# Kernel optimization log

Hardware: AMD Instinct MI355X
Metric: run time of the kernel (lower is better)

## Reference

```python
import jax, jax.numpy as jnp
import numpy as np


def setup_inputs() -> dict:
    key = jax.random.key(0)
    ks = jax.random.split(key, 6)
    B, N, F = 32, 1000, 256
    x = jax.random.normal(ks[0], (B, N, F), jnp.float32)
    num_nodes = jax.random.randint(ks[1], (B,), 500, N + 1, dtype=jnp.int32)
    num_sentences = jax.random.randint(ks[2], (B,), 10, 100, dtype=jnp.int32)
    valid = (jnp.arange(N)[None, :] < num_nodes[:, None]).astype(jnp.float32)
    # sparse-like weighted adjacency (avg degree ~20), zeroed on padded rows/cols
    w = jax.random.uniform(ks[3], (B, N, N), jnp.float32)
    m = (jax.random.uniform(ks[4], (B, N, N)) < 0.02).astype(jnp.float32)
    adj = w * m * valid[:, :, None] * valid[:, None, :]
    W = jax.random.normal(ks[5], (F, 1), jnp.float32) * 0.1
    b = jnp.zeros((1,), jnp.float32)
    return dict(x=x, adj=adj, W=W, b=b, num_nodes=num_nodes,
                num_sentences=num_sentences, num_output_sentences=3)


def reference(x, adj, W, b, num_nodes, num_sentences, num_output_sentences):
    B, N, F = x.shape
    I = jnp.eye(N, dtype=x.dtype)
    valid = jnp.arange(N)[None, :] < num_nodes[:, None]  # [B,N]

    # --- GCNConv attention: sym-normalized (A_bin + I), out dim 1 ---
    A_bin = (adj > 0).astype(x.dtype)
    A_hat = A_bin + I
    dis = A_hat.sum(-1) ** -0.5  # deg >= 1 from self loops
    norm = dis[:, :, None] * A_hat * dis[:, None, :]
    alpha = jnp.einsum('bnm,bmf,fo->bno', norm, x, W)[..., 0] + b[0]
    alpha = jax.nn.sigmoid(alpha ** 2)           # pow(.,2) then sigmoid
    alpha = jnp.where(valid, alpha, -1.0)        # padded nodes sort last, cut to 0

    # --- top-k cutoff: keep highest-alpha nodes until num_output_sentences
    # sentence nodes (node index < num_sentences) have been seen ---
    order = jnp.argsort(-alpha, axis=-1)                      # descending
    is_sent = (order < num_sentences[:, None]).astype(jnp.int32)
    cum = jnp.cumsum(is_sent, axis=-1)
    cut_pos = jnp.argmax(cum >= num_output_sentences, axis=-1)  # first hit
    cut_node = jnp.take_along_axis(order, cut_pos[:, None], axis=1)
    cut_value = jnp.take_along_axis(alpha, cut_node, axis=1)     # [B,1]
    cut_alpha = jax.nn.relu(alpha + 1e-7 - cut_value)
    rank_mask = (jnp.arange(N)[None, :] <= cut_pos[:, None]).astype(x.dtype)
    index_mask = jnp.zeros_like(alpha).at[jnp.arange(B)[:, None], order].set(rank_mask)

    # --- normalize_batch_adj on the weighted adjacency ---
    A2 = adj + I
    d2 = jnp.clip(A2.sum(-1), 1.0) ** -0.5
    normA = d2[:, :, None] * A2 * d2[:, None, :]
    normA = (adj.sum(-1) > 0).astype(x.dtype)[:, :, None] * normA

    # --- assignment matrix S = row-L1-normalized (normA * cut_alpha[cols]) ---
    S = normA * cut_alpha[:, None, :]
    S = S / jnp.clip(jnp.sum(jnp.abs(S), axis=-1, keepdims=True), 1e-12)

    # --- coarsen: x' = S^T x ; A' = floor(S^T A S * 1e4)/1e4 ---
    x_c = jnp.einsum('bni,bnf->bif', S, x)
    coarse_adj = jnp.einsum('bim,bmj->bij', jnp.einsum('bni,bnm->bim', S, adj), S)
    coarse_adj = jnp.floor(coarse_adj * 1e4) / 1e4
    return x_c, coarse_adj, S, index_mask
```

## Files before the change

kernel.cpp:

```cpp
#include <hip/hip_runtime.h>
#include <math.h>
#include <limits.h>

#define CAP 64
#define TPB 256
#define RPB 4
#define NMAX 1024

__device__ inline float waveSum(float v) {
#pragma unroll
  for (int o = 32; o > 0; o >>= 1) v += __shfl_down(v, o, 64);
  return v;
}

__global__ void k_y(const float* __restrict__ x, const float* __restrict__ W,
                    float* __restrict__ y, int N, int F, int BN) {
  int wave = threadIdx.x >> 6, lane = threadIdx.x & 63;
  int bn = blockIdx.x * RPB + wave;
  if (bn >= BN) return;
  const float4* xr = (const float4*)(x + (size_t)bn * F);
  const float4* W4 = (const float4*)W;
  int f4 = F >> 2;
  float p = 0.f;
  for (int i = lane; i < f4; i += 64) {
    float4 a = xr[i], w = W4[i];
    p += a.x * w.x + a.y * w.y + a.z * w.z + a.w * w.w;
  }
  for (int f = (f4 << 2) + lane; f < F; f += 64) p += x[(size_t)bn * F + f] * W[f];
  float s = waveSum(p);
  if (lane == 0) y[bn] = s;
}

__global__ void k_rowstats(const float* __restrict__ adj, int* __restrict__ rowCnt,
                           int* __restrict__ rowIdx, float* __restrict__ rowVal,
                           float* __restrict__ dis, float* __restrict__ d2,
                           float* __restrict__ wsum, int N) {
  int bn = blockIdx.x;
  const float* row = adj + (size_t)bn * N;
  __shared__ int scnt;
  __shared__ float sred[4];
  if (threadIdx.x == 0) scnt = 0;
  __syncthreads();
  float ls = 0.f;
  for (int j = threadIdx.x; j < N; j += TPB) {
    float v = row[j];
    ls += v;
    if (v > 0.f) {
      int p = atomicAdd(&scnt, 1);
      if (p < CAP) { rowIdx[(size_t)bn * CAP + p] = j; rowVal[(size_t)bn * CAP + p] = v; }
    }
  }
  float w = waveSum(ls);
  int wave = threadIdx.x >> 6, lane = threadIdx.x & 63;
  if (lane == 0) sred[wave] = w;
  __syncthreads();
  if (threadIdx.x == 0) {
    float s = sred[0] + sred[1] + sred[2] + sred[3];
    int c = scnt;
    rowCnt[bn] = c;
    dis[bn] = 1.f / sqrtf((float)(c + 1));
    wsum[bn] = s;
    d2[bn] = 1.f / sqrtf(fmaxf(s + 1.f, 1.f));
  }
}

__global__ void k_alpha(const float* __restrict__ adj, const int* __restrict__ rowCnt,
                        const int* __restrict__ rowIdx, const float* __restrict__ dis,
                        const float* __restrict__ y, const float* __restrict__ bptr,
                        const int* __restrict__ num_nodes, float* __restrict__ alpha,
                        int N, int BN) {
  int wave = threadIdx.x >> 6, lane = threadIdx.x & 63;
  int bn = blockIdx.x * 4 + wave;
  if (bn >= BN) return;
  int b = bn / N, n = bn - b * N;
  const float* disB = dis + (size_t)b * N;
  const float* yB = y + (size_t)b * N;
  int cnt = rowCnt[bn];
  float acc = 0.f;
  if (cnt <= CAP) {
    for (int t = lane; t < cnt; t += 64) {
      int j = rowIdx[(size_t)bn * CAP + t];
      acc += disB[j] * yB[j];
    }
  } else {
    const float* row = adj + (size_t)bn * N;
    for (int j = lane; j < N; j += 64)
      if (row[j] > 0.f) acc += disB[j] * yB[j];
  }
  float tot = waveSum(acc);
  if (lane == 0) {
    float dn = dis[bn];
    tot += dn * yB[n];
    float z = dn * tot + bptr[0];
    float a;
    if (n < num_nodes[b]) { float z2 = z * z; a = 1.f / (1.f + expf(-z2)); }
    else a = -1.f;
    alpha[bn] = a;
  }
}

__global__ void k_cut(const float* __restrict__ alpha, const int* __restrict__ num_sentences,
                      const int* __restrict__ kptr, float* __restrict__ cutA,
                      float* __restrict__ outIM, int* __restrict__ colK,
                      int* __restrict__ colIdx, int N) {
  int b = blockIdx.x;
  const float* aB = alpha + (size_t)b * N;
  __shared__ float s_cutv;
  __shared__ int s_cutn;
  if (threadIdx.x < 64) {
    int lane = threadIdx.x;
    int ns = num_sentences[b];
    int k = kptr[0];
    if (k < 1) k = 1;
    if (k > ns) k = ns;
    unsigned long long used = 0ULL;
    float cv = 0.f; int cn = 0;
    int nslots = (ns + 63) >> 6;
    for (int r = 0; r < k; r++) {
      float bv = -3.4e38f; int bi = INT_MAX;
      for (int s = 0; s < nslots; s++) {
        int idx = lane + (s << 6);
        if (idx < ns && !((used >> s) & 1ULL)) {
          float v = aB[idx];
          if (v > bv || (v == bv && idx < bi)) { bv = v; bi = idx; }
        }
      }
#pragma unroll
      for (int o = 32; o > 0; o >>= 1) {
        float ov = __shfl_down(bv, o, 64);
        int oi = __shfl_down(bi, o, 64);
        if (ov > bv || (ov == bv && oi < bi)) { bv = ov; bi = oi; }
      }
      bv = __shfl(bv, 0, 64);
      bi = __shfl(bi, 0, 64);
      if ((bi & 63) == lane) used |= 1ULL << (bi >> 6);
      cv = bv; cn = bi;
    }
    if (lane == 0) { s_cutv = cv; s_cutn = cn; }
  }
  __syncthreads();
  float cutv = s_cutv;
  int cutn = s_cutn;
  for (int n = threadIdx.x; n < N; n += TPB) {
    float a = aB[n];
    float ca = fmaxf((a + 1e-7f) - cutv, 0.f);
    cutA[(size_t)b * N + n] = ca;
    outIM[(size_t)b * N + n] = (a > cutv || (a == cutv && n <= cutn)) ? 1.f : 0.f;
    if (ca > 0.f) {
      int p = atomicAdd(&colK[b], 1);
      colIdx[(size_t)b * N + p] = n;
    }
  }
}

__global__ void k_srow(const float* __restrict__ adj, const int* __restrict__ rowCnt,
                       const int* __restrict__ rowIdx, const float* __restrict__ rowVal,
                       const float* __restrict__ wsum, const float* __restrict__ d2,
                       const float* __restrict__ cutA, float* __restrict__ outS,
                       int* __restrict__ colCount, int* __restrict__ colR,
                       float* __restrict__ colV, int N, int BN) {
  int wave = threadIdx.x >> 6, lane = threadIdx.x & 63;
  int bn = blockIdx.x * RPB + wave;
  bool rowOK = bn < BN;
  __shared__ float srow[RPB][NMAX];
  float* my = srow[wave];
  if (rowOK) for (int j = lane; j < N; j += 64) my[j] = 0.f;
  __syncthreads();
  if (rowOK && wsum[bn] > 0.f) {
    int b = bn / N, n = bn - b * N;
    int cnt = rowCnt[bn];
    const float* d2B = d2 + (size_t)b * N;
    const float* caB = cutA + (size_t)b * N;
    float d2n = d2[bn];
    if (cnt < CAP) {
      int t = lane;
      int j = -1; float a2 = 0.f;
      if (t < cnt) {
        j = rowIdx[(size_t)bn * CAP + t];
        float v = rowVal[(size_t)bn * CAP + t];
        a2 = v + (j == n ? 1.f : 0.f);
      }
      unsigned long long hasDiag = __ballot(t < cnt && j == n);
      if (t == cnt && hasDiag == 0ULL) { j = n; a2 = 1.f; }
      float sun = 0.f;
      if (j >= 0) {
        float ca = caB[j];
        if (ca > 0.f) sun = d2n * a2 * d2B[j] * ca;
        else j = -1;
      }
      float denom = __shfl(waveSum(sun), 0, 64);
      denom = fmaxf(denom, 1e-12f);
      if (j >= 0) {
        float s = sun / denom;
        my[j] = s;
        int cp = atomicAdd(&colCount[(size_t)b * N + j], 1);
        if (cp < CAP) {
          colR[((size_t)b * N + j) * CAP + cp] = n;
          colV[((size_t)b * N + j) * CAP + cp] = s;
        }
      }
    } else {
      const float* row = adj + (size_t)bn * N;
      float ls = 0.f;
      for (int j2 = lane; j2 < N; j2 += 64) {
        float v = row[j2];
        bool nz = (v > 0.f) || (j2 == n);
        float a2 = v + (j2 == n ? 1.f : 0.f);
        float ca = caB[j2];
        if (nz && ca > 0.f) ls += d2n * a2 * d2B[j2] * ca;
      }
      float denom = __shfl(waveSum(ls), 0, 64);
      denom = fmaxf(denom, 1e-12f);
      for (int j2 = lane; j2 < N; j2 += 64) {
        float v = row[j2];
        bool nz = (v > 0.f) || (j2 == n);
        float a2 = v + (j2 == n ? 1.f : 0.f);
        float ca = caB[j2];
        if (nz && ca > 0.f) {
          float s = (d2n * a2 * d2B[j2] * ca) / denom;
          my[j2] = s;
          int cp = atomicAdd(&colCount[(size_t)b * N + j2], 1);
          if (cp < CAP) {
            colR[((size_t)b * N + j2) * CAP + cp] = n;
            colV[((size_t)b * N + j2) * CAP + cp] = s;
          }
        }
      }
    }
  }
  __syncthreads();
  if (rowOK) {
    float* dst = outS + (size_t)bn * N;
    float4* d4 = (float4*)dst;
    int nq = N >> 2;
    for (int q = lane; q < nq; q += 64)
      d4[q] = make_float4(my[4 * q], my[4 * q + 1], my[4 * q + 2], my[4 * q + 3]);
    for (int j = (nq << 2) + lane; j < N; j += 64) dst[j] = my[j];
  }
}

__global__ void k_coarse(const float* __restrict__ adj, const float* __restrict__ x,
                         const float* __restrict__ cutA,
                         const int* __restrict__ rowCnt, const int* __restrict__ rowIdx,
                         const float* __restrict__ rowVal,
                         const int* __restrict__ colK, const int* __restrict__ colIdx,
                         const int* __restrict__ colCount, const int* __restrict__ colR,
                         const float* __restrict__ colV,
                         float* __restrict__ outXc, float* __restrict__ outC,
                         int N, int F) {
  int bn = blockIdx.x;
  int b = bn / N;
  float* xcRow = outXc + (size_t)bn * F;
  float* cRow = outC + (size_t)bn * N;
  int nq = N >> 2;
  if (cutA[bn] <= 0.f) {
    for (int f = threadIdx.x; f < F; f += TPB) xcRow[f] = 0.f;
    float4* d4 = (float4*)cRow;
    for (int q = threadIdx.x; q < nq; q += TPB) d4[q] = make_float4(0.f, 0.f, 0.f, 0.f);
    for (int j = (nq << 2) + threadIdx.x; j < N; j += TPB) cRow[j] = 0.f;
    return;
  }
  __shared__ float T[NMAX];
  __shared__ float crow[NMAX];
  __shared__ int eR[CAP];
  __shared__ float eV[CAP];
  __shared__ int eCnt[CAP];
  int cci = colCount[bn];
  if (cci > CAP) cci = CAP;
  for (int r = threadIdx.x; r < cci; r += TPB) {
    int n_r = colR[(size_t)bn * CAP + r];
    eR[r] = n_r;
    eV[r] = colV[(size_t)bn * CAP + r];
    eCnt[r] = rowCnt[(size_t)b * N + n_r];
  }
  for (int m = threadIdx.x; m < N; m += TPB) { T[m] = 0.f; crow[m] = 0.f; }
  __syncthreads();
  const float* xB = x + (size_t)b * N * F;
  for (int f = threadIdx.x; f < F; f += TPB) {
    float acc = 0.f;
    for (int r = 0; r < cci; r++) acc += eV[r] * xB[(size_t)eR[r] * F + f];
    xcRow[f] = acc;
  }
  for (int idx = threadIdx.x; idx < cci * CAP; idx += TPB) {
    int r = idx >> 6;
    int t = idx & (CAP - 1);
    int c = eCnt[r];
    if (c <= CAP && t < c) {
      size_t base = ((size_t)b * N + eR[r]) * CAP;
      atomicAdd(&T[rowIdx[base + t]], eV[r] * rowVal[base + t]);
    }
  }
  for (int r = 0; r < cci; r++) {
    if (eCnt[r] > CAP) {
      const float* arow = adj + ((size_t)b * N + eR[r]) * N;
      float v = eV[r];
      for (int m = threadIdx.x; m < N; m += TPB) {
        float a = arow[m];
        if (a != 0.f) atomicAdd(&T[m], v * a);
      }
    }
  }
  __syncthreads();
  int K = colK[b];
  for (int jj = threadIdx.x; jj < K; jj += TPB) {
    int j = colIdx[(size_t)b * N + jj];
    int cj = colCount[(size_t)b * N + j];
    if (cj > CAP) cj = CAP;
    const int* jR = colR + ((size_t)b * N + j) * CAP;
    const float* jV = colV + ((size_t)b * N + j) * CAP;
    float cc = 0.f;
    for (int p = 0; p < cj; p++) cc += T[jR[p]] * jV[p];
    crow[j] = floorf(cc * 1e4f) / 1e4f;
  }
  __syncthreads();
  float4* d4 = (float4*)cRow;
  for (int q = threadIdx.x; q < nq; q += TPB)
    d4[q] = make_float4(crow[4 * q], crow[4 * q + 1], crow[4 * q + 2], crow[4 * q + 3]);
  for (int j = (nq << 2) + threadIdx.x; j < N; j += TPB) cRow[j] = crow[j];
}

extern "C" void kernel_launch(void* const* d_in, const int* in_sizes, int n_in,
                              void* d_out, int out_size, void* d_ws, size_t ws_size,
                              hipStream_t stream) {
  const float* x = (const float*)d_in[0];
  const float* adj = (const float*)d_in[1];
  const float* W = (const float*)d_in[2];
  const float* bias = (const float*)d_in[3];
  const int* num_nodes = (const int*)d_in[4];
  const int* num_sentences = (const int*)d_in[5];
  const int* kptr = (const int*)d_in[6];

  int F = in_sizes[2];
  int B = in_sizes[4];
  int N = (int)(in_sizes[0] / ((long long)B * F));
  size_t BN = (size_t)B * N;

  float* outXc = (float*)d_out;
  float* outC = outXc + BN * F;
  float* outS = outC + BN * N;
  float* outIM = outS + BN * N;

  char* p = (char*)d_ws;
  auto alloc = [&](size_t bytes) -> void* {
    void* r = (void*)p;
    p += (bytes + 255) / 256 * 256;
    return r;
  };
  float* y = (float*)alloc(BN * 4);
  float* dis = (float*)alloc(BN * 4);
  float* d2 = (float*)alloc(BN * 4);
  float* wsum = (float*)alloc(BN * 4);
  float* alpha = (float*)alloc(BN * 4);
  float* cutA = (float*)alloc(BN * 4);
  int* rowCnt = (int*)alloc(BN * 4);
  int* rowIdx = (int*)alloc(BN * CAP * 4);
  float* rowVal = (float*)alloc(BN * CAP * 4);
  int* colCount = (int*)alloc(BN * 4);
  int* colR = (int*)alloc(BN * CAP * 4);
  float* colV = (float*)alloc(BN * CAP * 4);
  int* colK = (int*)alloc(B * 4);
  int* colIdx = (int*)alloc(BN * 4);

  hipMemsetAsync(colCount, 0, BN * 4, stream);
  hipMemsetAsync(colK, 0, B * 4, stream);

  int BNi = (int)BN;
  int rowBlocks = (BNi + RPB - 1) / RPB;
  k_y<<<dim3(rowBlocks), dim3(TPB), 0, stream>>>(x, W, y, N, F, BNi);
  k_rowstats<<<dim3(BNi), dim3(TPB), 0, stream>>>(adj, rowCnt, rowIdx, rowVal, dis, d2, wsum, N);
  k_alpha<<<dim3(rowBlocks), dim3(TPB), 0, stream>>>(adj, rowCnt, rowIdx, dis, y, bias,
                                                     num_nodes, alpha, N, BNi);
  k_cut<<<dim3(B), dim3(TPB), 0, stream>>>(alpha, num_sentences, kptr, cutA, outIM, colK, colIdx, N);
  k_srow<<<dim3(rowBlocks), dim3(TPB), 0, stream>>>(adj, rowCnt, rowIdx, rowVal, wsum, d2, cutA,
                                                    outS, colCount, colR, colV, N, BNi);
  k_coarse<<<dim3(BNi), dim3(TPB), 0, stream>>>(adj, x, cutA, rowCnt, rowIdx, rowVal,
                                                colK, colIdx, colCount, colR, colV,
                                                outXc, outC, N, F);
}
```

Before: 500.1 us.

## Fuse x·W projection and adjacency row stats into one wave-per-row kernel

Merges the x·W dot-product kernel and the adjacency row-statistics kernel into a single kernel that handles one row per wavefront, reading the adjacency row with float4 loads and counting nonzeros with per-wave shared atomics. The two memsets are folded into this kernel's prologue, and block-level __syncthreads are dropped in k_srow because each wave touches only its own shared row. This removes two launches, two memsets and a block-wide reduction per row. The cost is one wave per row instead of a 256-thread block during the adjacency scan.

```diff
diff --git a/kernel.cpp b/kernel.cpp
--- a/kernel.cpp
+++ b/kernel.cpp
@@ -13,50 +13,58 @@
   return v;
 }
 
-__global__ void k_y(const float* __restrict__ x, const float* __restrict__ W,
-                    float* __restrict__ y, int N, int F, int BN) {
+__global__ void k_prep(const float* __restrict__ x, const float* __restrict__ adj,
+                       const float* __restrict__ W, float* __restrict__ y,
+                       int* __restrict__ rowCnt, int* __restrict__ rowIdx,
+                       float* __restrict__ rowVal, float* __restrict__ dis,
+                       float* __restrict__ d2, float* __restrict__ wsum,
+                       int* __restrict__ colCount, int* __restrict__ colK,
+                       int N, int F, int BN, int B) {
+  __shared__ int scnt[RPB];
   int wave = threadIdx.x >> 6, lane = threadIdx.x & 63;
+  if (blockIdx.x == 0 && threadIdx.x < B) colK[threadIdx.x] = 0;
   int bn = blockIdx.x * RPB + wave;
   if (bn >= BN) return;
-  const float4* xr = (const float4*)(x + (size_t)bn * F);
-  const float4* W4 = (const float4*)W;
-  int f4 = F >> 2;
+  if (lane == 0) { scnt[wave] = 0; colCount_dummy: ; colCount[bn] = 0; }
   float p = 0.f;
-  for (int i = lane; i < f4; i += 64) {
-    float4 a = xr[i], w = W4[i];
-    p += a.x * w.x + a.y * w.y + a.z * w.z + a.w * w.w;
-  }
-  for (int f = (f4 << 2) + lane; f < F; f += 64) p += x[(size_t)bn * F + f] * W[f];
-  float s = waveSum(p);
-  if (lane == 0) y[bn] = s;
-}
-
-__global__ void k_rowstats(const float* __restrict__ adj, int* __restrict__ rowCnt,
-                           int* __restrict__ rowIdx, float* __restrict__ rowVal,
-                           float* __restrict__ dis, float* __restrict__ d2,
-                           float* __restrict__ wsum, int N) {
-  int bn = blockIdx.x;
+  if ((F & 3) == 0) {
+    const float4* xr = (const float4*)(x + (size_t)bn * F);
+    const float4* W4 = (const float4*)W;
+    int f4 = F >> 2;
+    for (int i = lane; i < f4; i += 64) {
+      float4 a = xr[i], w = W4[i];
+      p += a.x * w.x + a.y * w.y + a.z * w.z + a.w * w.w;
+    }
+  } else {
+    for (int f = lane; f < F; f += 64) p += x[(size_t)bn * F + f] * W[f];
+  }
+  float ydot = waveSum(p);
   const float* row = adj + (size_t)bn * N;
-  __shared__ int scnt;
-  __shared__ float sred[4];
-  if (threadIdx.x == 0) scnt = 0;
-  __syncthreads();
+  size_t lbase = (size_t)bn * CAP;
   float ls = 0.f;
-  for (int j = threadIdx.x; j < N; j += TPB) {
-    float v = row[j];
-    ls += v;
-    if (v > 0.f) {
-      int p = atomicAdd(&scnt, 1);
-      if (p < CAP) { rowIdx[(size_t)bn * CAP + p] = j; rowVal[(size_t)bn * CAP + p] = v; }
-    }
-  }
-  float w = waveSum(ls);
-  int wave = threadIdx.x >> 6, lane = threadIdx.x & 63;
-  if (lane == 0) sred[wave] = w;
-  __syncthreads();
-  if (threadIdx.x == 0) {
-    float s = sred[0] + sred[1] + sred[2] + sred[3];
-    int c = scnt;
+  if ((N & 3) == 0) {
+    const float4* r4 = (const float4*)row;
+    int n4 = N >> 2;
+    for (int q = lane; q < n4; q += 64) {
+      float4 v = r4[q];
+      ls += v.x + v.y + v.z + v.w;
+      int j = q << 2;
+      if (v.x > 0.f) { int pz = atomicAdd(&scnt[wave], 1); if (pz < CAP) { rowIdx[lbase + pz] = j;     rowVal[lbase + pz] = v.x; } }
+      if (v.y > 0.f) { int pz = atomicAdd(&scnt[wave], 1); if (pz < CAP) { rowIdx[lbase + pz] = j + 1; rowVal[lbase + pz] = v.y; } }
+      if (v.z > 0.f) { int pz = atomicAdd(&scnt[wave], 1); if (pz < CAP) { rowIdx[lbase + pz] = j + 2; rowVal[lbase + pz] = v.z; } }
+      if (v.w > 0.f) { int pz = atomicAdd(&scnt[wave], 1); if (pz < CAP) { rowIdx[lbase + pz] = j + 3; rowVal[lbase + pz] = v.w; } }
+    }
+  } else {
+    for (int j = lane; j < N; j += 64) {
+      float v = row[j];
+      ls += v;
+      if (v > 0.f) { int pz = atomicAdd(&scnt[wave], 1); if (pz < CAP) { rowIdx[lbase + pz] = j; rowVal[lbase + pz] = v; } }
+    }
+  }
+  float s = waveSum(ls);
+  if (lane == 0) {
+    y[bn] = ydot;
+    int c = scnt[wave];
     rowCnt[bn] = c;
     dis[bn] = 1.f / sqrtf((float)(c + 1));
     wsum[bn] = s;
@@ -70,7 +78,7 @@
                         const int* __restrict__ num_nodes, float* __restrict__ alpha,
                         int N, int BN) {
   int wave = threadIdx.x >> 6, lane = threadIdx.x & 63;
-  int bn = blockIdx.x * 4 + wave;
+  int bn = blockIdx.x * RPB + wave;
   if (bn >= BN) return;
   int b = bn / N, n = bn - b * N;
   const float* disB = dis + (size_t)b * N;
@@ -165,7 +173,6 @@
   __shared__ float srow[RPB][NMAX];
   float* my = srow[wave];
   if (rowOK) for (int j = lane; j < N; j += 64) my[j] = 0.f;
-  __syncthreads();
   if (rowOK && wsum[bn] > 0.f) {
     int b = bn / N, n = bn - b * N;
     int cnt = rowCnt[bn];
@@ -228,14 +235,16 @@
       }
     }
   }
-  __syncthreads();
   if (rowOK) {
     float* dst = outS + (size_t)bn * N;
-    float4* d4 = (float4*)dst;
-    int nq = N >> 2;
-    for (int q = lane; q < nq; q += 64)
-      d4[q] = make_float4(my[4 * q], my[4 * q + 1], my[4 * q + 2], my[4 * q + 3]);
-    for (int j = (nq << 2) + lane; j < N; j += 64) dst[j] = my[j];
+    if ((N & 3) == 0) {
+      float4* d4 = (float4*)dst;
+      int nq = N >> 2;
+      for (int q = lane; q < nq; q += 64)
+        d4[q] = make_float4(my[4 * q], my[4 * q + 1], my[4 * q + 2], my[4 * q + 3]);
+    } else {
+      for (int j = lane; j < N; j += 64) dst[j] = my[j];
+    }
   }
 }
 
@@ -252,12 +261,14 @@
   int b = bn / N;
   float* xcRow = outXc + (size_t)bn * F;
   float* cRow = outC + (size_t)bn * N;
-  int nq = N >> 2;
+  bool v4N = (N & 3) == 0, v4F = (F & 3) == 0;
+  int nq = N >> 2, fq = F >> 2;
   if (cutA[bn] <= 0.f) {
-    for (int f = threadIdx.x; f < F; f += TPB) xcRow[f] = 0.f;
-    float4* d4 = (float4*)cRow;
-    for (int q = threadIdx.x; q < nq; q += TPB) d4[q] = make_float4(0.f, 0.f, 0.f, 0.f);
-    for (int j = (nq << 2) + threadIdx.x; j < N; j += TPB) cRow[j] = 0.f;
+    float4 z4 = make_float4(0.f, 0.f, 0.f, 0.f);
+    if (v4F) { float4* x4 = (float4*)xcRow; for (int q = threadIdx.x; q < fq; q += TPB) x4[q] = z4; }
+    else for (int f = threadIdx.x; f < F; f += TPB) xcRow[f] = 0.f;
+    if (v4N) { float4* d4 = (float4*)cRow; for (int q = threadIdx.x; q < nq; q += TPB) d4[q] = z4; }
+    else for (int j = threadIdx.x; j < N; j += TPB) cRow[j] = 0.f;
     return;
   }
   __shared__ float T[NMAX];
@@ -313,10 +324,13 @@
     crow[j] = floorf(cc * 1e4f) / 1e4f;
   }
   __syncthreads();
-  float4* d4 = (float4*)cRow;
-  for (int q = threadIdx.x; q < nq; q += TPB)
-    d4[q] = make_float4(crow[4 * q], crow[4 * q + 1], crow[4 * q + 2], crow[4 * q + 3]);
-  for (int j = (nq << 2) + threadIdx.x; j < N; j += TPB) cRow[j] = crow[j];
+  if (v4N) {
+    float4* d4 = (float4*)cRow;
+    for (int q = threadIdx.x; q < nq; q += TPB)
+      d4[q] = make_float4(crow[4 * q], crow[4 * q + 1], crow[4 * q + 2], crow[4 * q + 3]);
+  } else {
+    for (int j = threadIdx.x; j < N; j += TPB) cRow[j] = crow[j];
+  }
 }
 
 extern "C" void kernel_launch(void* const* d_in, const int* in_sizes, int n_in,
@@ -361,13 +375,10 @@
   int* colK = (int*)alloc(B * 4);
   int* colIdx = (int*)alloc(BN * 4);
 
-  hipMemsetAsync(colCount, 0, BN * 4, stream);
-  hipMemsetAsync(colK, 0, B * 4, stream);
-
   int BNi = (int)BN;
   int rowBlocks = (BNi + RPB - 1) / RPB;
-  k_y<<<dim3(rowBlocks), dim3(TPB), 0, stream>>>(x, W, y, N, F, BNi);
-  k_rowstats<<<dim3(BNi), dim3(TPB), 0, stream>>>(adj, rowCnt, rowIdx, rowVal, dis, d2, wsum, N);
+  k_prep<<<dim3(rowBlocks), dim3(TPB), 0, stream>>>(x, adj, W, y, rowCnt, rowIdx, rowVal,
+                                                    dis, d2, wsum, colCount, colK, N, F, BNi, B);
   k_alpha<<<dim3(rowBlocks), dim3(TPB), 0, stream>>>(adj, rowCnt, rowIdx, dis, y, bias,
                                                      num_nodes, alpha, N, BNi);
   k_cut<<<dim3(B), dim3(TPB), 0, stream>>>(alpha, num_sentences, kptr, cutA, outIM, colK, colIdx, N);
```

Result: faster. 477.5 us (-4.5%).
